# Optimization experiments

Hardware: AMD Instinct MI355X
Metric: run time of the kernel (lower is better)

## Reference

```python
import jax, jax.numpy as jnp
import numpy as np

B, T, C = 2, 2048, 2048
H = 16
D = C // H  # head_size = 128
ROPE_BASE = 10000.0


def _rope_cos_sin(seq_len, dim, dtype=jnp.float32):
    # torchtune RotaryPositionalEmbeddings: interleaved pair rotation
    inv_freq = 1.0 / (ROPE_BASE ** (jnp.arange(0, dim, 2, dtype=jnp.float32) / dim))  # [D/2]
    ang = jnp.arange(seq_len, dtype=jnp.float32)[:, None] * inv_freq[None, :]  # [T, D/2]
    return jnp.cos(ang).astype(dtype), jnp.sin(ang).astype(dtype)


def _apply_rope(x, cos, sin):
    # x: [B, T, H, D]; rotate interleaved pairs (even, odd)
    x1 = x[..., 0::2]
    x2 = x[..., 1::2]
    c = cos[None, :, None, :]
    s = sin[None, :, None, :]
    out = jnp.stack([x1 * c - x2 * s, x1 * s + x2 * c], axis=-1)  # [B,T,H,D/2,2]
    return out.reshape(x.shape)


def setup_inputs() -> dict:
    key = jax.random.key(0)
    ks = jax.random.split(key, 5)
    scale = 1.0 / np.sqrt(C)
    return {
        "x": jax.random.normal(ks[0], (B, T, C), jnp.float32),
        "W_attn": jax.random.normal(ks[1], (C, 3 * C), jnp.float32) * scale,
        "b_attn": jax.random.normal(ks[2], (3 * C,), jnp.float32) * 0.01,
        "W_proj": jax.random.normal(ks[3], (C, C), jnp.float32) * scale,
        "b_proj": jax.random.normal(ks[4], (C,), jnp.float32) * 0.01,
    }


def reference(x, W_attn, b_attn, W_proj, b_proj):
    b, t, c = x.shape
    qkv = x @ W_attn + b_attn                      # [B,T,3C]
    q, k, v = jnp.split(qkv, 3, axis=-1)
    q = q.reshape(b, t, H, D)
    k = k.reshape(b, t, H, D)
    v = v.reshape(b, t, H, D)
    cos, sin = _rope_cos_sin(t, D, x.dtype)
    q = _apply_rope(q, cos, sin)
    k = _apply_rope(k, cos, sin)
    # [B,H,T,D]
    q = q.transpose(0, 2, 1, 3)
    k = k.transpose(0, 2, 1, 3)
    v = v.transpose(0, 2, 1, 3)
    scores = jnp.einsum("bhqd,bhkd->bhqk", q, k) / jnp.sqrt(jnp.asarray(D, x.dtype))
    causal = jnp.tril(jnp.ones((t, t), dtype=bool))  # [T,T]
    scores = jnp.where(causal[None, None], scores, jnp.asarray(-jnp.inf, scores.dtype))
    probs = jax.nn.softmax(scores, axis=-1)
    out = jnp.einsum("bhqk,bhkd->bhqd", probs, v)  # [B,H,T,D]
    out = out.transpose(0, 2, 1, 3).reshape(b, t, c)
    return out @ W_proj + b_proj
```

## Files before the change

### kernel.cpp

```cpp
#include <hip/hip_runtime.h>
#include <hip/hip_bf16.h>
#include <math.h>

#define B_ 2
#define T_ 2048
#define C_ 2048
#define H_ 16
#define D_ 128
#define M_ (B_ * T_)
#define N3C (3 * C_)

typedef __attribute__((ext_vector_type(8))) short v8s;
typedef __attribute__((ext_vector_type(4))) float v4f;

typedef const __attribute__((address_space(1))) void* gas_t;
typedef __attribute__((address_space(3))) void* las_t;

__device__ __forceinline__ void gl16(const void* g, void* l) {
  __builtin_amdgcn_global_load_lds((gas_t)g, (las_t)l, 16, 0, 0);
}

__device__ inline unsigned short f2bf(float f) {
  unsigned u = __builtin_bit_cast(unsigned, f);
  u += 0x7FFFu + ((u >> 16) & 1u);
  return (unsigned short)(u >> 16);
}
__device__ inline float bf2f(unsigned short h) {
  unsigned u = (unsigned)h << 16;
  return __builtin_bit_cast(float, u);
}

__global__ __launch_bounds__(256) void split_rows(
    const float* __restrict__ X, unsigned short* __restrict__ XH,
    unsigned short* __restrict__ XL) {
  const long i4 = ((long)blockIdx.x * 256 + threadIdx.x) * 4;
  float4 v = *(const float4*)(X + i4);
  ushort4 hh, ll;
  hh.x = f2bf(v.x); ll.x = f2bf(v.x - bf2f(hh.x));
  hh.y = f2bf(v.y); ll.y = f2bf(v.y - bf2f(hh.y));
  hh.z = f2bf(v.z); ll.z = f2bf(v.z - bf2f(hh.z));
  hh.w = f2bf(v.w); ll.w = f2bf(v.w - bf2f(hh.w));
  *(ushort4*)&XH[i4] = hh;
  *(ushort4*)&XL[i4] = ll;
}

__global__ __launch_bounds__(256) void convert_wT(
    const float* __restrict__ W, unsigned short* __restrict__ WH,
    unsigned short* __restrict__ WL, int K, int N) {
  __shared__ float Ts[64][68];
  const int tid = threadIdx.x;
  const int n0 = blockIdx.x * 64;
  const int k0 = blockIdx.y * 64;
#pragma unroll
  for (int it = 0; it < 4; ++it) {
    int f = it * 256 + tid;
    int r = f >> 4;
    int c4 = (f & 15) * 4;
    float4 v = *(const float4*)(W + (long)(k0 + r) * N + n0 + c4);
    *(float4*)&Ts[r][c4] = v;
  }
  __syncthreads();
#pragma unroll
  for (int it = 0; it < 4; ++it) {
    int f = it * 256 + tid;
    int rn = f >> 4;
    int c4 = (f & 15) * 4;
    float x0 = Ts[c4 + 0][rn];
    float x1 = Ts[c4 + 1][rn];
    float x2 = Ts[c4 + 2][rn];
    float x3 = Ts[c4 + 3][rn];
    ushort4 hh, ll;
    hh.x = f2bf(x0); ll.x = f2bf(x0 - bf2f(hh.x));
    hh.y = f2bf(x1); ll.y = f2bf(x1 - bf2f(hh.y));
    hh.z = f2bf(x2); ll.z = f2bf(x2 - bf2f(hh.z));
    hh.w = f2bf(x3); ll.w = f2bf(x3 - bf2f(hh.w));
    long o = (long)(n0 + rn) * K + k0 + c4;
    *(ushort4*)&WH[o] = hh;
    *(ushort4*)&WL[o] = ll;
  }
}

__global__ __launch_bounds__(256) void gemm_pre_mfma(
    const unsigned short* __restrict__ AH, const unsigned short* __restrict__ AL,
    const unsigned short* __restrict__ BH, const unsigned short* __restrict__ BL,
    const float* __restrict__ bias, float* __restrict__ C, int K, int N) {
  __shared__ unsigned short smem[4 * 4096];
  unsigned short* sAH = smem;
  unsigned short* sAL = smem + 4096;
  unsigned short* sBH = smem + 8192;
  unsigned short* sBL = smem + 12288;

  const int tid = threadIdx.x;
  const int lane = tid & 63;
  const int w = tid >> 6;
  const int lm = lane & 15;
  const int quad = lane >> 4;

  const int gx = gridDim.x;
  const int lin = blockIdx.y * gx + blockIdx.x;
  const int pid_m = (lin & 7) + ((lin >> 3) / gx) * 8;
  const int pid_n = (lin >> 3) % gx;
  const int bm = pid_m * 128;
  const int bn = pid_n * 128;

  const int wm = (w & 1) * 64;
  const int wn = (w >> 1) * 64;

  const int srow = 32 * w + (lane >> 2);
  const int scol = (lane & 3) * 8;
  const unsigned short* pAH0 = AH + (size_t)(bm + srow) * K + scol;
  const unsigned short* pAH1 = pAH0 + (size_t)16 * K;
  const unsigned short* pAL0 = AL + (size_t)(bm + srow) * K + scol;
  const unsigned short* pAL1 = pAL0 + (size_t)16 * K;
  const unsigned short* pBH0 = BH + (size_t)(bn + srow) * K + scol;
  const unsigned short* pBH1 = pBH0 + (size_t)16 * K;
  const unsigned short* pBL0 = BL + (size_t)(bn + srow) * K + scol;
  const unsigned short* pBL1 = pBL0 + (size_t)16 * K;
  unsigned short* dAH = sAH + 1024 * w;
  unsigned short* dAL = sAL + 1024 * w;
  unsigned short* dBH = sBH + 1024 * w;
  unsigned short* dBL = sBL + 1024 * w;

  v4f acc[4][4];
#pragma unroll
  for (int i = 0; i < 4; ++i)
#pragma unroll
    for (int j = 0; j < 4; ++j) {
      v4f z = {0.f, 0.f, 0.f, 0.f};
      acc[i][j] = z;
    }

  for (int k0 = 0; k0 < K; k0 += 32) {
    __syncthreads();
    gl16(pAH0, dAH);
    gl16(pAH1, dAH + 512);
    gl16(pAL0, dAL);
    gl16(pAL1, dAL + 512);
    gl16(pBH0, dBH);
    gl16(pBH1, dBH + 512);
    gl16(pBL0, dBL);
    gl16(pBL1, dBL + 512);
    pAH0 += 32; pAH1 += 32; pAL0 += 32; pAL1 += 32;
    pBH0 += 32; pBH1 += 32; pBL0 += 32; pBL1 += 32;
    __syncthreads();

    v8s aH[4], aL[4], bHf[4], bLf[4];
#pragma unroll
    for (int mt = 0; mt < 4; ++mt) {
      const int r = wm + mt * 16 + lm;
      aH[mt] = *(const v8s*)&sAH[r * 32 + quad * 8];
      aL[mt] = *(const v8s*)&sAL[r * 32 + quad * 8];
    }
#pragma unroll
    for (int nt = 0; nt < 4; ++nt) {
      const int r = wn + nt * 16 + lm;
      bHf[nt] = *(const v8s*)&sBH[r * 32 + quad * 8];
      bLf[nt] = *(const v8s*)&sBL[r * 32 + quad * 8];
    }
#pragma unroll
    for (int mt = 0; mt < 4; ++mt)
#pragma unroll
      for (int nt = 0; nt < 4; ++nt) {
        acc[mt][nt] = __builtin_amdgcn_mfma_f32_16x16x32_bf16(aH[mt], bHf[nt], acc[mt][nt], 0, 0, 0);
        acc[mt][nt] = __builtin_amdgcn_mfma_f32_16x16x32_bf16(aH[mt], bLf[nt], acc[mt][nt], 0, 0, 0);
        acc[mt][nt] = __builtin_amdgcn_mfma_f32_16x16x32_bf16(aL[mt], bHf[nt], acc[mt][nt], 0, 0, 0);
      }
  }

  __syncthreads();
  float* eps = (float*)smem;
  float* myeps = eps + w * 1088;

  float bv[4];
#pragma unroll
  for (int nt = 0; nt < 4; ++nt) bv[nt] = bias[bn + wn + nt * 16 + lm];

  const int r2 = lane >> 2;
  const int c4 = (lane & 3) * 4;
#pragma unroll
  for (int mt = 0; mt < 4; ++mt) {
#pragma unroll
    for (int nt = 0; nt < 4; ++nt)
#pragma unroll
      for (int r = 0; r < 4; ++r)
        myeps[(quad * 4 + r) * 68 + nt * 16 + lm] = acc[mt][nt][r] + bv[nt];
    float* dst = C + (size_t)(bm + wm + mt * 16 + r2) * N + bn + wn + c4;
#pragma unroll
    for (int i = 0; i < 4; ++i) {
      float4 v = *(float4*)&myeps[r2 * 68 + c4 + i * 16];
      *(float4*)&dst[i * 16] = v;
    }
  }
}

__global__ __launch_bounds__(256) void rope_split(
    const float* __restrict__ qkv,
    unsigned short* __restrict__ QH, unsigned short* __restrict__ QL,
    unsigned short* __restrict__ KH, unsigned short* __restrict__ KL,
    unsigned short* __restrict__ VTH, unsigned short* __restrict__ VTL) {
  const int tb = blockIdx.x;
  const int h = blockIdx.y;
  const int b = blockIdx.z;
  const int tid = threadIdx.x;

  __shared__ unsigned short VH_s[128][66];
  __shared__ unsigned short VL_s[128][66];

  for (int part = 0; part < 2; ++part) {
    unsigned short* OH = part ? KH : QH;
    unsigned short* OL = part ? KL : QL;
    const float sc = part ? 1.0f : 0.12751879523595298f;
    const size_t colbase = (size_t)part * C_ + (size_t)h * D_;
#pragma unroll 2
    for (int it = 0; it < 16; ++it) {
      int f = it * 256 + tid;
      int r = f >> 6;
      int i = f & 63;
      int t = tb * 64 + r;
      float inv = exp2f(-(float)i * (13.28771237954945f / 64.0f));
      float ang = (float)t * inv;
      float s, c;
      sincosf(ang, &s, &c);
      const float* src = qkv + (size_t)(b * T_ + t) * N3C + colbase + 2 * i;
      float2 x = *(const float2*)src;
      float ox = (x.x * c - x.y * s) * sc;
      float oy = (x.x * s + x.y * c) * sc;
      size_t dst = ((size_t)(b * H_ + h) * T_ + t) * D_ + 2 * i;
      unsigned short hx = f2bf(ox), hy = f2bf(oy);
      ushort2 hh; hh.x = hx; hh.y = hy;
      *(ushort2*)&OH[dst] = hh;
      ushort2 ll; ll.x = f2bf(ox - bf2f(hx)); ll.y = f2bf(oy - bf2f(hy));
      *(ushort2*)&OL[dst] = ll;
    }
  }

#pragma unroll
  for (int it = 0; it < 8; ++it) {
    int f = it * 256 + tid;
    int r = f >> 5;
    int d4 = (f & 31) * 4;
    float4 v = *(const float4*)(qkv + (size_t)(b * T_ + tb * 64 + r) * N3C + 2 * C_ + h * D_ + d4);
    float vv[4] = {v.x, v.y, v.z, v.w};
#pragma unroll
    for (int j = 0; j < 4; ++j) {
      unsigned short hi = f2bf(vv[j]);
      VH_s[d4 + j][r] = hi;
      VL_s[d4 + j][r] = f2bf(vv[j] - bf2f(hi));
    }
  }
  __syncthreads();
#pragma unroll
  for (int it = 0; it < 4; ++it) {
    int f = it * 256 + tid;
    int d = f >> 3;
    int c8 = (f & 7) * 8;
    size_t dst = ((size_t)(b * H_ + h) * D_ + d) * T_ + tb * 64 + c8;
    unsigned short th[8], tl[8];
#pragma unroll
    for (int j = 0; j < 8; ++j) { th[j] = VH_s[d][c8 + j]; tl[j] = VL_s[d][c8 + j]; }
    *(uint4*)&VTH[dst] = *(uint4*)th;
    *(uint4*)&VTL[dst] = *(uint4*)tl;
  }
}

__global__ __launch_bounds__(512, 4) void attn_mfma(
    const unsigned short* __restrict__ QH, const unsigned short* __restrict__ QL,
    const unsigned short* __restrict__ KH, const unsigned short* __restrict__ KL,
    const unsigned short* __restrict__ VTH, const unsigned short* __restrict__ VTL,
    unsigned short* __restrict__ OHp, unsigned short* __restrict__ OLp) {
  const int qb = (int)gridDim.x - 1 - (int)blockIdx.x;
  const int h = blockIdx.y;
  const int b = blockIdx.z;
  const int tid = threadIdx.x;
  const int lane = tid & 63;
  const int w = tid >> 6;
  const int lm = lane & 15;
  const int quad = lane >> 4;

  __shared__ unsigned short KS_H[32][136], KS_L[32][136];
  __shared__ unsigned short VS_H[128][40], VS_L[128][40];
  __shared__ unsigned short PS_H[128][40], PS_L[128][40];

  const size_t qbase = ((size_t)(b * H_ + h) * T_ + qb * 128 + w * 16 + lm) * D_;
  v8s qh[4], ql[4];
#pragma unroll
  for (int ks = 0; ks < 4; ++ks) {
    qh[ks] = *(const v8s*)&QH[qbase + ks * 32 + quad * 8];
    ql[ks] = *(const v8s*)&QL[qbase + ks * 32 + quad * 8];
  }

  v8s ones;
#pragma unroll
  for (int j = 0; j < 8; ++j) ones[j] = (short)0x3F80;

  const int kr = tid >> 4;
  const int kc = (tid & 15) * 8;
  const int vd = tid >> 2;
  const int vc = (tid & 3) * 8;

  const size_t kbase0 = (size_t)(b * H_ + h) * T_ * D_;
  const size_t vbase0 = (size_t)(b * H_ + h) * D_ * T_;
  const int nkb = 4 * qb + 4;

  uint4 khp = *(const uint4*)&KH[kbase0 + (size_t)kr * D_ + kc];
  uint4 klp = *(const uint4*)&KL[kbase0 + (size_t)kr * D_ + kc];
  uint4 vhp = *(const uint4*)&VTH[vbase0 + (size_t)vd * T_ + vc];
  uint4 vlp = *(const uint4*)&VTL[vbase0 + (size_t)vd * T_ + vc];

  v4f acc_o[8], acc_l;
#pragma unroll
  for (int nt = 0; nt < 8; ++nt) {
    v4f z = {0.f, 0.f, 0.f, 0.f};
    acc_o[nt] = z;
  }
  {
    v4f z = {0.f, 0.f, 0.f, 0.f};
    acc_l = z;
  }

  const float M2 = 32.0f;

  for (int kb = 0; kb < nkb; ++kb) {
    __syncthreads();
    *(uint4*)&KS_H[kr][kc] = khp;
    *(uint4*)&KS_L[kr][kc] = klp;
    *(uint4*)&VS_H[vd][vc] = vhp;
    *(uint4*)&VS_L[vd][vc] = vlp;
    __syncthreads();

    if (kb + 1 < nkb) {
      size_t kg = kbase0 + (size_t)((kb + 1) * 32 + kr) * D_ + kc;
      khp = *(const uint4*)&KH[kg];
      klp = *(const uint4*)&KL[kg];
      size_t vg = vbase0 + (size_t)vd * T_ + (kb + 1) * 32 + vc;
      vhp = *(const uint4*)&VTH[vg];
      vlp = *(const uint4*)&VTL[vg];
    }

    v4f s0, s1;
    {
      v4f z = {0.f, 0.f, 0.f, 0.f};
      s0 = z; s1 = z;
    }
#pragma unroll
    for (int ks = 0; ks < 4; ++ks) {
      int k8 = ks * 32 + quad * 8;
      v8s bh0 = *(const v8s*)&KS_H[lm][k8];
      v8s bl0 = *(const v8s*)&KS_L[lm][k8];
      v8s bh1 = *(const v8s*)&KS_H[16 + lm][k8];
      v8s bl1 = *(const v8s*)&KS_L[16 + lm][k8];
      s0 = __builtin_amdgcn_mfma_f32_16x16x32_bf16(qh[ks], bh0, s0, 0, 0, 0);
      s1 = __builtin_amdgcn_mfma_f32_16x16x32_bf16(qh[ks], bh1, s1, 0, 0, 0);
      s0 = __builtin_amdgcn_mfma_f32_16x16x32_bf16(qh[ks], bl0, s0, 0, 0, 0);
      s1 = __builtin_amdgcn_mfma_f32_16x16x32_bf16(qh[ks], bl1, s1, 0, 0, 0);
      s0 = __builtin_amdgcn_mfma_f32_16x16x32_bf16(ql[ks], bh0, s0, 0, 0, 0);
      s1 = __builtin_amdgcn_mfma_f32_16x16x32_bf16(ql[ks], bh1, s1, 0, 0, 0);
    }

#pragma unroll
    for (int r = 0; r < 4; ++r) {
      int rowg = qb * 128 + w * 16 + quad * 4 + r;
      float v0 = (kb * 32 + lm > rowg) ? -INFINITY : s0[r];
      float v1 = (kb * 32 + 16 + lm > rowg) ? -INFINITY : s1[r];
      float p0 = __builtin_amdgcn_exp2f(v0 - M2);
      float p1 = __builtin_amdgcn_exp2f(v1 - M2);

      int prow = w * 16 + quad * 4 + r;
      unsigned short p0h = f2bf(p0);
      PS_H[prow][lm] = p0h;
      PS_L[prow][lm] = f2bf(p0 - bf2f(p0h));
      unsigned short p1h = f2bf(p1);
      PS_H[prow][16 + lm] = p1h;
      PS_L[prow][16 + lm] = f2bf(p1 - bf2f(p1h));
    }

    v8s ph = *(const v8s*)&PS_H[w * 16 + lm][quad * 8];
    v8s pl = *(const v8s*)&PS_L[w * 16 + lm][quad * 8];
    acc_l = __builtin_amdgcn_mfma_f32_16x16x32_bf16(ph, ones, acc_l, 0, 0, 0);
    acc_l = __builtin_amdgcn_mfma_f32_16x16x32_bf16(pl, ones, acc_l, 0, 0, 0);
#pragma unroll
    for (int nt = 0; nt < 8; ++nt) {
      v8s vh = *(const v8s*)&VS_H[nt * 16 + lm][quad * 8];
      v8s vl = *(const v8s*)&VS_L[nt * 16 + lm][quad * 8];
      acc_o[nt] = __builtin_amdgcn_mfma_f32_16x16x32_bf16(ph, vh, acc_o[nt], 0, 0, 0);
      acc_o[nt] = __builtin_amdgcn_mfma_f32_16x16x32_bf16(ph, vl, acc_o[nt], 0, 0, 0);
      acc_o[nt] = __builtin_amdgcn_mfma_f32_16x16x32_bf16(pl, vh, acc_o[nt], 0, 0, 0);
    }
  }

#pragma unroll
  for (int r = 0; r < 4; ++r) {
    float invl = 1.0f / acc_l[r];
    size_t row = (size_t)(b * T_ + qb * 128 + w * 16 + quad * 4 + r);
#pragma unroll
    for (int nt = 0; nt < 8; ++nt) {
      float o = acc_o[nt][r] * invl;
      unsigned short oh = f2bf(o);
      size_t idx = row * C_ + h * D_ + nt * 16 + lm;
      OHp[idx] = oh;
      OLp[idx] = f2bf(o - bf2f(oh));
    }
  }
}

extern "C" void kernel_launch(void* const* d_in, const int* in_sizes, int n_in,
                              void* d_out, int out_size, void* d_ws, size_t ws_size,
                              hipStream_t stream) {
  const float* x      = (const float*)d_in[0];
  const float* W_attn = (const float*)d_in[1];
  const float* b_attn = (const float*)d_in[2];
  const float* W_proj = (const float*)d_in[3];
  const float* b_proj = (const float*)d_in[4];
  float* out = (float*)d_out;

  char* wsb = (char*)d_ws;
  const size_t MiB = 1048576;
  float* qkv = (float*)wsb;
  unsigned short* WtaH = (unsigned short*)(wsb + 96 * MiB);
  unsigned short* WtaL = (unsigned short*)(wsb + 120 * MiB);
  unsigned short* XH   = (unsigned short*)(wsb + 144 * MiB);
  unsigned short* XL   = (unsigned short*)(wsb + 160 * MiB);
  unsigned short* QH   = (unsigned short*)(wsb + 96 * MiB);
  unsigned short* QL   = (unsigned short*)(wsb + 112 * MiB);
  unsigned short* KH   = (unsigned short*)(wsb + 128 * MiB);
  unsigned short* KL   = (unsigned short*)(wsb + 144 * MiB);
  unsigned short* VTH  = (unsigned short*)(wsb + 160 * MiB);
  unsigned short* VTL  = (unsigned short*)(wsb + 176 * MiB);
  unsigned short* WtpH = (unsigned short*)(wsb + 32 * MiB);
  unsigned short* WtpL = (unsigned short*)(wsb + 40 * MiB);
  unsigned short* AOH  = (unsigned short*)(wsb + 48 * MiB);
  unsigned short* AOL  = (unsigned short*)(wsb + 64 * MiB);

  convert_wT<<<dim3(N3C / 64, C_ / 64), 256, 0, stream>>>(W_attn, WtaH, WtaL, C_, N3C);
  split_rows<<<dim3((M_ * C_) / 1024), 256, 0, stream>>>(x, XH, XL);
  gemm_pre_mfma<<<dim3(N3C / 128, M_ / 128), 256, 0, stream>>>(
      XH, XL, WtaH, WtaL, b_attn, qkv, C_, N3C);
  rope_split<<<dim3(T_ / 64, H_, B_), 256, 0, stream>>>(qkv, QH, QL, KH, KL, VTH, VTL);
  convert_wT<<<dim3(C_ / 64, C_ / 64), 256, 0, stream>>>(W_proj, WtpH, WtpL, C_, C_);
  attn_mfma<<<dim3(T_ / 128, H_, B_), 512, 0, stream>>>(
      QH, QL, KH, KL, VTH, VTL, AOH, AOL);
  gemm_pre_mfma<<<dim3(C_ / 128, M_ / 128), 256, 0, stream>>>(
      AOH, AOL, WtpH, WtpL, b_proj, out, C_, C_);
}
```

Baseline: 768.3 us.

## Double-buffer LDS tiles in split-bf16 GEMM with XOR swizzle and MFMA priority

The GEMM now keeps two LDS stages. It issues the next K-tile's global_load_lds transfers before running the MFMAs on the current tile, so global loads overlap with matrix math instead of being fully exposed behind a barrier every iteration. The 16-byte chunk positions in each row are XOR-swizzled on both write and read to reduce LDS bank conflicts. s_setprio is raised around the MFMA block. This doubles the kernel's LDS footprint, which may reduce occupancy.

```diff
diff --git a/kernel.cpp b/kernel.cpp
--- a/kernel.cpp
+++ b/kernel.cpp
@@ -84,11 +84,7 @@
     const unsigned short* __restrict__ AH, const unsigned short* __restrict__ AL,
     const unsigned short* __restrict__ BH, const unsigned short* __restrict__ BL,
     const float* __restrict__ bias, float* __restrict__ C, int K, int N) {
-  __shared__ unsigned short smem[4 * 4096];
-  unsigned short* sAH = smem;
-  unsigned short* sAL = smem + 4096;
-  unsigned short* sBH = smem + 8192;
-  unsigned short* sBL = smem + 12288;
+  __shared__ unsigned short smem[2 * 4 * 4096];
 
   const int tid = threadIdx.x;
   const int lane = tid & 63;
@@ -107,7 +103,7 @@
   const int wn = (w >> 1) * 64;
 
   const int srow = 32 * w + (lane >> 2);
-  const int scol = (lane & 3) * 8;
+  const int scol = ((lane & 3) ^ ((lane >> 3) & 3)) * 8;
   const unsigned short* pAH0 = AH + (size_t)(bm + srow) * K + scol;
   const unsigned short* pAH1 = pAH0 + (size_t)16 * K;
   const unsigned short* pAL0 = AL + (size_t)(bm + srow) * K + scol;
@@ -116,10 +112,19 @@
   const unsigned short* pBH1 = pBH0 + (size_t)16 * K;
   const unsigned short* pBL0 = BL + (size_t)(bn + srow) * K + scol;
   const unsigned short* pBL1 = pBL0 + (size_t)16 * K;
-  unsigned short* dAH = sAH + 1024 * w;
-  unsigned short* dAL = sAL + 1024 * w;
-  unsigned short* dBH = sBH + 1024 * w;
-  unsigned short* dBL = sBL + 1024 * w;
+
+#define STAGE(base, kk) do {                                      \
+    unsigned short* d_ = (base) + 1024 * w;                       \
+    const int ko_ = (kk) * 32;                                    \
+    gl16(pAH0 + ko_, d_);                                         \
+    gl16(pAH1 + ko_, d_ + 512);                                   \
+    gl16(pAL0 + ko_, d_ + 4096);                                  \
+    gl16(pAL1 + ko_, d_ + 4096 + 512);                            \
+    gl16(pBH0 + ko_, d_ + 8192);                                  \
+    gl16(pBH1 + ko_, d_ + 8192 + 512);                            \
+    gl16(pBL0 + ko_, d_ + 12288);                                 \
+    gl16(pBL1 + ko_, d_ + 12288 + 512);                           \
+  } while (0)
 
   v4f acc[4][4];
 #pragma unroll
@@ -130,33 +135,39 @@
       acc[i][j] = z;
     }
 
-  for (int k0 = 0; k0 < K; k0 += 32) {
+  const int kswz = (quad ^ ((lm >> 1) & 3)) * 8;
+
+  const int nk = K >> 5;
+  unsigned short* sb = smem;
+  unsigned short* nb = smem + 16384;
+
+  STAGE(sb, 0);
+
+  for (int t = 0; t < nk; ++t) {
     __syncthreads();
-    gl16(pAH0, dAH);
-    gl16(pAH1, dAH + 512);
-    gl16(pAL0, dAL);
-    gl16(pAL1, dAL + 512);
-    gl16(pBH0, dBH);
-    gl16(pBH1, dBH + 512);
-    gl16(pBL0, dBL);
-    gl16(pBL1, dBL + 512);
-    pAH0 += 32; pAH1 += 32; pAL0 += 32; pAL1 += 32;
-    pBH0 += 32; pBH1 += 32; pBL0 += 32; pBL1 += 32;
-    __syncthreads();
+
+    if (t + 1 < nk) STAGE(nb, t + 1);
+
+    const unsigned short* sAH = sb;
+    const unsigned short* sAL = sb + 4096;
+    const unsigned short* sBH = sb + 8192;
+    const unsigned short* sBL = sb + 12288;
 
     v8s aH[4], aL[4], bHf[4], bLf[4];
 #pragma unroll
     for (int mt = 0; mt < 4; ++mt) {
       const int r = wm + mt * 16 + lm;
-      aH[mt] = *(const v8s*)&sAH[r * 32 + quad * 8];
-      aL[mt] = *(const v8s*)&sAL[r * 32 + quad * 8];
+      aH[mt] = *(const v8s*)&sAH[r * 32 + kswz];
+      aL[mt] = *(const v8s*)&sAL[r * 32 + kswz];
     }
 #pragma unroll
     for (int nt = 0; nt < 4; ++nt) {
       const int r = wn + nt * 16 + lm;
-      bHf[nt] = *(const v8s*)&sBH[r * 32 + quad * 8];
-      bLf[nt] = *(const v8s*)&sBL[r * 32 + quad * 8];
-    }
+      bHf[nt] = *(const v8s*)&sBH[r * 32 + kswz];
+      bLf[nt] = *(const v8s*)&sBL[r * 32 + kswz];
+    }
+
+    __builtin_amdgcn_s_setprio(1);
 #pragma unroll
     for (int mt = 0; mt < 4; ++mt)
 #pragma unroll
@@ -165,7 +176,11 @@
         acc[mt][nt] = __builtin_amdgcn_mfma_f32_16x16x32_bf16(aH[mt], bLf[nt], acc[mt][nt], 0, 0, 0);
         acc[mt][nt] = __builtin_amdgcn_mfma_f32_16x16x32_bf16(aL[mt], bHf[nt], acc[mt][nt], 0, 0, 0);
       }
-  }
+    __builtin_amdgcn_s_setprio(0);
+
+    unsigned short* tmp = sb; sb = nb; nb = tmp;
+  }
+#undef STAGE
 
   __syncthreads();
   float* eps = (float*)smem;
```

Result: faster. 740.3 us (-3.6%).
